# Kernel tuning notes

Measured on AMD Instinct MI355X. Metric: run time of the kernel, lower is better.

## Reference

```python
import jax, jax.numpy as jnp
import numpy as np

VAR_NUM = 96
EMBED_TIME = 128
INPUT_DIM = VAR_NUM * 2 + EMBED_TIME  # 320
ATTN_DIM = 64
N_HEADS = 8
ALL_DIM = ATTN_DIM * N_HEADS  # 512
B, N = 8, 2048
NEG_INF = -1e9  # finite stand-in for masked_fill(-inf); safe under softmax


def setup_inputs() -> dict:
    key = jax.random.key(0)
    ks = jax.random.split(key, 16)
    s = lambda d: 1.0 / np.sqrt(d)
    return {
        "times_in": jax.random.uniform(ks[0], (B, N), jnp.float32),
        "data_in": jax.random.normal(ks[1], (B, N, VAR_NUM), jnp.float32),
        "mask_in": jnp.ones((B, N, VAR_NUM), jnp.float32),
        "exist_times": jax.random.randint(ks[2], (B, N), 0, 2, jnp.int32),
        # TimeEmbedding params
        "w_per": jax.random.normal(ks[3], (1, EMBED_TIME - 1), jnp.float32),
        "b_per": jnp.zeros((EMBED_TIME - 1,), jnp.float32),
        "w_lin": jax.random.normal(ks[4], (1, 1), jnp.float32),
        "b_lin": jnp.zeros((1,), jnp.float32),
        # Attention params
        "Wq": jax.random.normal(ks[5], (INPUT_DIM, ALL_DIM), jnp.float32) * s(INPUT_DIM),
        "bq": jnp.zeros((ALL_DIM,), jnp.float32),
        "Wk": jax.random.normal(ks[6], (INPUT_DIM, ALL_DIM), jnp.float32) * s(INPUT_DIM),
        "bk": jnp.zeros((ALL_DIM,), jnp.float32),
        "Wv": jax.random.normal(ks[7], (INPUT_DIM, ALL_DIM), jnp.float32) * s(INPUT_DIM),
        "bv": jnp.zeros((ALL_DIM,), jnp.float32),
        "Wfc": jax.random.normal(ks[8], (ALL_DIM, ATTN_DIM), jnp.float32) * s(ALL_DIM),
        "bfc": jnp.zeros((ATTN_DIM,), jnp.float32),
    }


def reference(times_in, data_in, mask_in, exist_times,
              w_per, b_per, w_lin, b_lin,
              Wq, bq, Wk, bk, Wv, bv, Wfc, bfc):
    b, n = times_in.shape
    tt = times_in[..., None]  # [b, n, 1]
    # TimeEmbedding: [linear(tt), sin(periodic(tt))]
    te = jnp.concatenate([tt @ w_lin + b_lin, jnp.sin(tt @ w_per + b_per)], axis=-1)
    x = jnp.concatenate([data_in, mask_in, te], axis=-1)  # [b, n, INPUT_DIM]

    def heads(w, bias):
        return (x @ w + bias).reshape(b, n, N_HEADS, ATTN_DIM).transpose(0, 2, 1, 3)

    q, k, v = heads(Wq, bq), heads(Wk, bk), heads(Wv, bv)  # [b, h, n, d]
    # NOTE: custom scale uses sqrt(input_dim), not sqrt(head_dim)
    scores = jnp.einsum("bhqd,bhkd->bhqk", q, k) / jnp.sqrt(jnp.float32(INPUT_DIM))
    m = (exist_times != 0)
    scores = jnp.where(m[:, None, None, :], scores, NEG_INF)  # mask keys
    attn = jax.nn.softmax(scores, axis=-1)  # dropout p=0 in eval reference
    out = jnp.einsum("bhqk,bhkd->bhqd", attn, v)
    out = jnp.where(m[:, None, :, None], out, 0.0)  # zero masked query rows
    out = out.transpose(0, 2, 1, 3).reshape(b, n, ALL_DIM)
    return out @ Wfc + bfc  # [b, n, ATTN_DIM]
```

## Files before the change

### kernel.cpp

```cpp
#include <hip/hip_runtime.h>

#define N_ 2048
#define BN 16384
#define IN_DIM 320
#define QKV_N 1536
#define ALPHA 0.08064911f

typedef float f32x4 __attribute__((ext_vector_type(4)));
typedef short v8s __attribute__((ext_vector_type(8)));
typedef unsigned int u32x2 __attribute__((ext_vector_type(2)));

__device__ __forceinline__ short f2b(float f) {
  unsigned u = __builtin_bit_cast(unsigned, f);
  u = u + 0x7fff + ((u >> 16) & 1);
  return (short)(u >> 16);
}

__device__ __forceinline__ int piperm(int t) {
  return ((t >> 5) & 1) * 32 + ((t >> 2) & 3) * 8 + ((t >> 4) & 1) * 4 + (t & 3);
}

__device__ __forceinline__ size_t fragaddr(int ti, int r, int k) {
  return (size_t)ti * 512 + ((k >> 3) & 3) * 128 + r * 8 + (k & 7);
}

__global__ void build_x(const float* __restrict__ times, const float* __restrict__ data,
                        const float* __restrict__ maskv, const float* __restrict__ w_per,
                        const float* __restrict__ b_per, const float* __restrict__ w_lin,
                        const float* __restrict__ b_lin, short* __restrict__ xF) {
  int row = blockIdx.x;
  int t = threadIdx.x;
  float tt = times[row];
  int rt = row >> 4, l16r = row & 15;
  const float* dr = data + (size_t)row * 96;
  const float* mr = maskv + (size_t)row * 96;
  if (t < 96) {
    xF[fragaddr(rt * 10 + (t >> 5), l16r, t & 31)] = f2b(dr[t]);
    int k2 = 96 + t;
    xF[fragaddr(rt * 10 + (k2 >> 5), l16r, k2 & 31)] = f2b(mr[t]);
  }
  float val;
  if (t == 0) val = tt * w_lin[0] + b_lin[0];
  else        val = __sinf(tt * w_per[t - 1] + b_per[t - 1]);
  int k3 = 192 + t;
  xF[fragaddr(rt * 10 + (k3 >> 5), l16r, k3 & 31)] = f2b(val);
}

__global__ void scan_mask(const int* __restrict__ exist, int* __restrict__ prefix,
                          int* __restrict__ ntg, int* __restrict__ totals,
                          short* __restrict__ flagsc) {
  __shared__ int sums[256];
  int b = blockIdx.x;
  int t = threadIdx.x;
  const int* e = exist + b * 2048;
  int loc[8];
  int s = 0;
#pragma unroll
  for (int j = 0; j < 8; ++j) { loc[j] = s; s += (e[t * 8 + j] != 0) ? 1 : 0; }
  sums[t] = s;
  __syncthreads();
  for (int d = 1; d < 256; d <<= 1) {
    int v = (t >= d) ? sums[t - d] : 0;
    __syncthreads();
    sums[t] += v;
    __syncthreads();
  }
  int total = sums[255];
  int base = (t == 0) ? 0 : sums[t - 1];
#pragma unroll
  for (int j = 0; j < 8; ++j) prefix[b * 2048 + t * 8 + j] = base + loc[j];
  if (t == 0) { ntg[b] = (total + 63) >> 6; totals[b] = total; }
#pragma unroll
  for (int j = 0; j < 8; ++j) {
    int slot = t * 8 + j;
    flagsc[b * 2048 + (slot & ~63) + piperm(slot & 63)] =
        (slot < total) ? (short)0x3F80 : (short)0;
  }
}

__global__ void transpose_w(const float* __restrict__ Wq, const float* __restrict__ Wk,
                            const float* __restrict__ Wv, const float* __restrict__ Wfc,
                            short* __restrict__ WtF, short* __restrict__ WfcT) {
  int idx = blockIdx.x * 256 + threadIdx.x;
  if (idx < QKV_N * IN_DIM) {
    int n = idx / IN_DIM, kk = idx - n * IN_DIM;
    const float* W = (n < 512) ? Wq : (n < 1024 ? Wk : Wv);
    WtF[fragaddr((n >> 4) * 10 + (kk >> 5), n & 15, kk & 31)] =
        f2b(W[(size_t)kk * 512 + (n & 511)]);
  } else {
    int j = idx - QKV_N * IN_DIM;
    int d = j >> 9, kk = j & 511;
    WfcT[j] = f2b(Wfc[kk * 64 + d]);
  }
}

__launch_bounds__(256)
__global__ void qkv_gemm(const short* __restrict__ xF, const short* __restrict__ WtF,
                         const float* __restrict__ bq, const float* __restrict__ bk,
                         const float* __restrict__ bv, const int* __restrict__ exist,
                         const int* __restrict__ prefix,
                         short* __restrict__ q, short* __restrict__ kc, short* __restrict__ vc) {
  int bm = blockIdx.x;
  int bn = blockIdx.y;
  int tid = threadIdx.x, wave = tid >> 6, lane = tid & 63;
  int wm = wave >> 1, wn = wave & 1;
  int l16 = lane & 15, lh = lane >> 4;
  int voff = lane * 8;
  const short* ap = xF + (size_t)(bm * 8 + wm * 4) * 10 * 512;
  const short* bp = WtF + (size_t)(bn * 8 + wn * 4) * 10 * 512;
  f32x4 acc[4][4] = {};
  v8s af[4], bfr[4];
#pragma unroll
  for (int m = 0; m < 4; ++m) af[m] = *(const v8s*)&ap[(size_t)(m * 10) * 512 + voff];
#pragma unroll
  for (int n = 0; n < 4; ++n) bfr[n] = *(const v8s*)&bp[(size_t)(n * 10) * 512 + voff];
#pragma unroll 1
  for (int kt = 0; kt < 10; ++kt) {
#pragma unroll
    for (int m = 0; m < 4; ++m)
#pragma unroll
      for (int n = 0; n < 4; ++n)
        acc[m][n] = __builtin_amdgcn_mfma_f32_16x16x32_bf16(af[m], bfr[n], acc[m][n], 0, 0, 0);
    if (kt < 9) {
#pragma unroll
      for (int m = 0; m < 4; ++m) af[m] = *(const v8s*)&ap[(size_t)(m * 10 + kt + 1) * 512 + voff];
#pragma unroll
      for (int n = 0; n < 4; ++n) bfr[n] = *(const v8s*)&bp[(size_t)(n * 10 + kt + 1) * 512 + voff];
    }
  }
  int w = bn >> 2;
  if (w == 0) {
#pragma unroll
    for (int m = 0; m < 4; ++m) {
      int row0 = bm * 128 + wm * 64 + m * 16 + lh * 4;
#pragma unroll
      for (int n = 0; n < 4; ++n) {
        int c = (bn * 128 + wn * 64 + n * 16 + l16) & 511;
        float bb = bq[c];
        int h = c >> 6, d = c & 63;
#pragma unroll
        for (int r = 0; r < 4; ++r) {
          int rr = row0 + r;
          int b = rr >> 11, ntok = rr & 2047;
          q[(((size_t)(b * 8 + h) * N_ + ntok) << 6) + d] = f2b((acc[m][n][r] + bb) * ALPHA);
        }
      }
    }
  } else {
    short* dbuf = (w == 1) ? kc : vc;
    const float* bias = (w == 1) ? bk : bv;
#pragma unroll
    for (int m = 0; m < 4; ++m) {
      int row0 = bm * 128 + wm * 64 + m * 16 + lh * 4;
      int exr[4], dstr[4];
#pragma unroll
      for (int r = 0; r < 4; ++r) { exr[r] = exist[row0 + r]; dstr[r] = prefix[row0 + r]; }
      int b = row0 >> 11;
#pragma unroll
      for (int n = 0; n < 4; ++n) {
        int c = (bn * 128 + wn * 64 + n * 16 + l16) & 511;
        float bb = bias[c];
        int h = c >> 6, d = c & 63;
#pragma unroll
        for (int r = 0; r < 4; ++r)
          if (exr[r])
            dbuf[(((size_t)(b * 8 + h) * N_ + dstr[r]) << 6) + d] = f2b(acc[m][n][r] + bb);
      }
    }
  }
}

__launch_bounds__(256)
__global__ void fragmentize(short* __restrict__ kc, short* __restrict__ vc,
                            const int* __restrict__ ntg, const int* __restrict__ totals) {
  __shared__ short Ks[64][66];
  __shared__ short Vs[64][66];
  int bh = blockIdx.x;
  int b = bh >> 3;
  int nt = ntg[b], total = totals[b];
  int tid = threadIdx.x;
  size_t hb = (size_t)bh * N_ * 64;
  for (int tile = blockIdx.y; tile < nt; tile += 8) {
    int base = tile * 64;
#pragma unroll
    for (int s = 0; s < 2; ++s) {
      int c = tid + s * 256, r = c >> 3, c8 = c & 7;
      v8s kv = {0, 0, 0, 0, 0, 0, 0, 0};
      v8s vv = {0, 0, 0, 0, 0, 0, 0, 0};
      if (base + r < total) {
        kv = *(const v8s*)&kc[hb + (size_t)(base + r) * 64 + c8 * 8];
        vv = *(const v8s*)&vc[hb + (size_t)(base + r) * 64 + c8 * 8];
      }
      *(v8s*)&Ks[r][c8 * 8] = kv;
      *(v8s*)&Vs[r][c8 * 8] = vv;
    }
    __syncthreads();
#pragma unroll
    for (int s = 0; s < 2; ++s) {
      int c = tid + s * 256;
      int i = c >> 6, lh2 = (c >> 4) & 3, r16 = c & 15;
      *(v8s*)&kc[hb + (size_t)tile * 4096 + c * 8] =
          *(const v8s*)&Ks[(i >> 1) * 16 + r16][(i & 1) * 32 + lh2 * 8];
      int l16 = c & 15, lh = (c >> 4) & 3, kc2 = (c >> 6) & 1, n2 = c >> 7;
      int d = n2 * 16 + l16;
      v8s o;
#pragma unroll
      for (int jj = 0; jj < 8; ++jj) {
        int t2 = kc2 * 32 + (jj >> 2) * 16 + lh * 4 + (jj & 3);
        o[jj] = Vs[t2][d];
      }
      *(v8s*)&vc[hb + (size_t)tile * 4096 + c * 8] = o;
    }
    __syncthreads();
  }
}

__launch_bounds__(256, 2)
__global__ void attn_kernel(const short* __restrict__ q, const short* __restrict__ kT,
                            const short* __restrict__ vT, const short* __restrict__ flagsc,
                            const int* __restrict__ ntg, const int* __restrict__ exist,
                            short* __restrict__ att) {
  int bx = blockIdx.x;
  int bh = ((bx >> 6) << 3) | (bx & 7);
  int qblk = (bx >> 3) & 7;
  int b = bh >> 3, h = bh & 7;
  int tid = threadIdx.x, wave = tid >> 6, lane = tid & 63;
  int l16 = lane & 15, lh = lane >> 4;
  int q0 = qblk * 256 + wave * 64;
  int nt = ntg[b];
  const short* qp = q + (size_t)bh * N_ * 64;
  const short* kpt = kT + (size_t)bh * 131072;
  const short* vpt = vT + (size_t)bh * 131072;
  const short* fpt = flagsc + b * N_;
  const int* ex = exist + b * N_;
  v8s qf[4][2];
#pragma unroll
  for (int m = 0; m < 4; ++m)
#pragma unroll
    for (int kcx = 0; kcx < 2; ++kcx)
      qf[m][kcx] = *(const v8s*)&qp[(size_t)(q0 + m * 16 + l16) * 64 + kcx * 32 + lh * 8];
  f32x4 oacc[4][4] = {};
  f32x4 lacc[4] = {};
  const f32x4 zf = {0.f, 0.f, 0.f, 0.f};
  int voff = lane * 8;
  v8s kf[8], vf[8], ff[2];
#pragma unroll
  for (int i = 0; i < 8; ++i) {
    kf[i] = *(const v8s*)&kpt[i * 512 + voff];
    vf[i] = *(const v8s*)&vpt[i * 512 + voff];
  }
  ff[0] = *(const v8s*)&fpt[lh * 8];
  ff[1] = *(const v8s*)&fpt[32 + lh * 8];
#pragma unroll 1
  for (int kt = 0; kt < nt; ++kt) {
    const short* kn = kpt + (size_t)(kt + 1) * 4096;
    const short* vn = vpt + (size_t)(kt + 1) * 4096;
    const short* fn = fpt + (kt + 1) * 64;
    bool pre = (kt + 1 < nt);
#pragma unroll
    for (int mh = 0; mh < 2; ++mh) {
      f32x4 sacc[2][4];
#pragma unroll
      for (int n = 0; n < 4; ++n)
#pragma unroll
        for (int mm = 0; mm < 2; ++mm) {
          sacc[mm][n] = __builtin_amdgcn_mfma_f32_16x16x32_bf16(kf[n * 2], qf[mh * 2 + mm][0], zf, 0, 0, 0);
          sacc[mm][n] = __builtin_amdgcn_mfma_f32_16x16x32_bf16(kf[n * 2 + 1], qf[mh * 2 + mm][1], sacc[mm][n], 0, 0, 0);
        }
      if (mh == 1 && pre)
#pragma unroll
        for (int i = 0; i < 8; ++i) kf[i] = *(const v8s*)&kn[i * 512 + voff];
      v8s pf[2][2];
#pragma unroll
      for (int mm = 0; mm < 2; ++mm)
#pragma unroll
        for (int kcx = 0; kcx < 2; ++kcx)
#pragma unroll
          for (int half = 0; half < 2; ++half) {
            int n = kcx * 2 + half;
            float p0 = __builtin_amdgcn_exp2f(sacc[mm][n][0]);
            float p1 = __builtin_amdgcn_exp2f(sacc[mm][n][1]);
            float p2 = __builtin_amdgcn_exp2f(sacc[mm][n][2]);
            float p3 = __builtin_amdgcn_exp2f(sacc[mm][n][3]);
            uint w0, w1;
            asm("v_cvt_pk_bf16_f32 %0, %1, %2" : "=v"(w0) : "v"(p0), "v"(p1));
            asm("v_cvt_pk_bf16_f32 %0, %1, %2" : "=v"(w1) : "v"(p2), "v"(p3));
            ((uint*)&pf[mm][kcx])[half * 2]     = w0;
            ((uint*)&pf[mm][kcx])[half * 2 + 1] = w1;
          }
#pragma unroll
      for (int kcx = 0; kcx < 2; ++kcx) {
#pragma unroll
        for (int mm = 0; mm < 2; ++mm)
          lacc[mh * 2 + mm] = __builtin_amdgcn_mfma_f32_16x16x32_bf16(pf[mm][kcx], ff[kcx], lacc[mh * 2 + mm], 0, 0, 0);
#pragma unroll
        for (int n = 0; n < 4; ++n)
#pragma unroll
          for (int mm = 0; mm < 2; ++mm)
            oacc[mh * 2 + mm][n] = __builtin_amdgcn_mfma_f32_16x16x32_bf16(pf[mm][kcx], vf[n * 2 + kcx], oacc[mh * 2 + mm][n], 0, 0, 0);
      }
    }
    if (pre) {
#pragma unroll
      for (int i = 0; i < 8; ++i) vf[i] = *(const v8s*)&vn[i * 512 + voff];
      ff[0] = *(const v8s*)&fn[lh * 8];
      ff[1] = *(const v8s*)&fn[32 + lh * 8];
    }
  }
#pragma unroll
  for (int m = 0; m < 4; ++m)
#pragma unroll
    for (int r = 0; r < 4; ++r) {
      int row = q0 + m * 16 + lh * 4 + r;
      float qm = (ex[row] != 0) ? 1.f : 0.f;
      float inv = qm / fmaxf(lacc[m][r], 1e-20f);
#pragma unroll
      for (int n = 0; n < 4; ++n)
        att[((size_t)(b * N_ + row)) * 512 + h * 64 + n * 16 + l16] = f2b(oacc[m][n][r] * inv);
    }
}

__launch_bounds__(256)
__global__ void out_gemm(const short* __restrict__ att, const short* __restrict__ WfcT,
                         const float* __restrict__ bfc, float* __restrict__ out) {
  __shared__ short As[128][40];
  __shared__ short Bs[64][40];
  int bm = blockIdx.x;
  int tid = threadIdx.x, wave = tid >> 6, lane = tid & 63;
  int l16 = lane & 15, lh = lane >> 4;
  f32x4 acc[2][4] = {};
  for (int kt = 0; kt < 16; ++kt) {
    int k0 = kt * 32;
#pragma unroll
    for (int s = 0; s < 2; ++s) {
      int c = tid + s * 256;
      int r = c >> 2, c8 = c & 3;
      *(v8s*)&As[r][c8 * 8] = *(const v8s*)&att[(size_t)(bm * 128 + r) * 512 + k0 + c8 * 8];
    }
    { int r = tid >> 2, c8 = tid & 3;
      if (r < 64) *(v8s*)&Bs[r][c8 * 8] = *(const v8s*)&WfcT[(size_t)r * 512 + k0 + c8 * 8]; }
    __syncthreads();
    v8s bfr[4];
#pragma unroll
    for (int n = 0; n < 4; ++n) bfr[n] = *(const v8s*)&Bs[n * 16 + l16][lh * 8];
#pragma unroll
    for (int m = 0; m < 2; ++m) {
      v8s af = *(const v8s*)&As[wave * 32 + m * 16 + l16][lh * 8];
#pragma unroll
      for (int n = 0; n < 4; ++n)
        acc[m][n] = __builtin_amdgcn_mfma_f32_16x16x32_bf16(af, bfr[n], acc[m][n], 0, 0, 0);
    }
    __syncthreads();
  }
#pragma unroll
  for (int m = 0; m < 2; ++m)
#pragma unroll
    for (int n = 0; n < 4; ++n) {
      float bb = bfc[n * 16 + l16];
#pragma unroll
      for (int r = 0; r < 4; ++r) {
        int row = bm * 128 + wave * 32 + m * 16 + lh * 4 + r;
        out[(size_t)row * 64 + n * 16 + l16] = acc[m][n][r] + bb;
      }
    }
}

extern "C" void kernel_launch(void* const* d_in, const int* in_sizes, int n_in,
                              void* d_out, int out_size, void* d_ws, size_t ws_size,
                              hipStream_t stream) {
  const float* times = (const float*)d_in[0];
  const float* data  = (const float*)d_in[1];
  const float* maskv = (const float*)d_in[2];
  const int*   exist = (const int*)d_in[3];
  const float* w_per = (const float*)d_in[4];
  const float* b_per = (const float*)d_in[5];
  const float* w_lin = (const float*)d_in[6];
  const float* b_lin = (const float*)d_in[7];
  const float* Wq  = (const float*)d_in[8];
  const float* bq  = (const float*)d_in[9];
  const float* Wk  = (const float*)d_in[10];
  const float* bk  = (const float*)d_in[11];
  const float* Wv  = (const float*)d_in[12];
  const float* bv  = (const float*)d_in[13];
  const float* Wfc = (const float*)d_in[14];
  const float* bfc = (const float*)d_in[15];
  float* out = (float*)d_out;

  char* ws = (char*)d_ws;
  short* xF    = (short*)(ws);
  short* WtF   = (short*)(ws + 10485760);
  short* WfcT  = (short*)(ws + 11468800);
  short* qb    = (short*)(ws + 11534336);
  short* kcb   = (short*)(ws + 28311552);
  short* vcb   = (short*)(ws + 45088768);
  short* att   = (short*)(ws + 61865984);
  short* flagsc= (short*)(ws + 78643200);
  int*   prefix= (int*)(ws + 78675968);
  int*   ntg   = (int*)(ws + 78741504);
  int*   totals= (int*)(ws + 78741536);

  build_x<<<BN, 128, 0, stream>>>(times, data, maskv, w_per, b_per, w_lin, b_lin, xF);
  scan_mask<<<8, 256, 0, stream>>>(exist, prefix, ntg, totals, flagsc);
  transpose_w<<<2048, 256, 0, stream>>>(Wq, Wk, Wv, Wfc, WtF, WfcT);
  qkv_gemm<<<dim3(128, 12), 256, 0, stream>>>(xF, WtF, bq, bk, bv, exist, prefix, qb, kcb, vcb);
  fragmentize<<<dim3(64, 8), 256, 0, stream>>>(kcb, vcb, ntg, totals);
  attn_kernel<<<512, 256, 0, stream>>>(qb, kcb, vcb, flagsc, ntg, exist, att);
  out_gemm<<<128, 256, 0, stream>>>(att, WfcT, bfc, out);
}
```

Baseline: 109.6 us.

## Compact existing rows before K/V GEMM and drop key-flag vectors in attention

build_x now also writes a compacted copy of the input rows, placed using the prefix scan, so the K/V projection GEMM runs only over existing tokens. Row blocks past each batch's valid count exit early, which removes roughly the masked fraction of K/V projection work and the scattered prefix/exist lookups in its epilogue. The attention kernel no longer loads per-tile flag vectors: it computes the row sum with a constant ones vector and subtracts the padding count from the denominator. This relies on padded K/V slots being zeroed later, so each pad contributes exactly exp2(0)=1 to the sum. The compacted buffer reuses the att workspace region, and scan_mask must now run before build_x.

```diff
diff --git a/kernel.cpp b/kernel.cpp
--- a/kernel.cpp
+++ b/kernel.cpp
@@ -24,31 +24,8 @@
   return (size_t)ti * 512 + ((k >> 3) & 3) * 128 + r * 8 + (k & 7);
 }
 
-__global__ void build_x(const float* __restrict__ times, const float* __restrict__ data,
-                        const float* __restrict__ maskv, const float* __restrict__ w_per,
-                        const float* __restrict__ b_per, const float* __restrict__ w_lin,
-                        const float* __restrict__ b_lin, short* __restrict__ xF) {
-  int row = blockIdx.x;
-  int t = threadIdx.x;
-  float tt = times[row];
-  int rt = row >> 4, l16r = row & 15;
-  const float* dr = data + (size_t)row * 96;
-  const float* mr = maskv + (size_t)row * 96;
-  if (t < 96) {
-    xF[fragaddr(rt * 10 + (t >> 5), l16r, t & 31)] = f2b(dr[t]);
-    int k2 = 96 + t;
-    xF[fragaddr(rt * 10 + (k2 >> 5), l16r, k2 & 31)] = f2b(mr[t]);
-  }
-  float val;
-  if (t == 0) val = tt * w_lin[0] + b_lin[0];
-  else        val = __sinf(tt * w_per[t - 1] + b_per[t - 1]);
-  int k3 = 192 + t;
-  xF[fragaddr(rt * 10 + (k3 >> 5), l16r, k3 & 31)] = f2b(val);
-}
-
 __global__ void scan_mask(const int* __restrict__ exist, int* __restrict__ prefix,
-                          int* __restrict__ ntg, int* __restrict__ totals,
-                          short* __restrict__ flagsc) {
+                          int* __restrict__ ntg, int* __restrict__ totals) {
   __shared__ int sums[256];
   int b = blockIdx.x;
   int t = threadIdx.x;
@@ -70,12 +47,42 @@
 #pragma unroll
   for (int j = 0; j < 8; ++j) prefix[b * 2048 + t * 8 + j] = base + loc[j];
   if (t == 0) { ntg[b] = (total + 63) >> 6; totals[b] = total; }
-#pragma unroll
-  for (int j = 0; j < 8; ++j) {
-    int slot = t * 8 + j;
-    flagsc[b * 2048 + (slot & ~63) + piperm(slot & 63)] =
-        (slot < total) ? (short)0x3F80 : (short)0;
-  }
+}
+
+__global__ void build_x(const float* __restrict__ times, const float* __restrict__ data,
+                        const float* __restrict__ maskv, const float* __restrict__ w_per,
+                        const float* __restrict__ b_per, const float* __restrict__ w_lin,
+                        const float* __restrict__ b_lin, const int* __restrict__ exist,
+                        const int* __restrict__ prefix,
+                        short* __restrict__ xF, short* __restrict__ xFc) {
+  int row = blockIdx.x;
+  int t = threadIdx.x;
+  float tt = times[row];
+  int rt = row >> 4, l16r = row & 15;
+  int b = row >> 11;
+  int dst = prefix[row];
+  bool ex = exist[row] != 0;
+  int tcb = (b * 128 + (dst >> 4)) * 10;
+  int l16c = dst & 15;
+  const float* dr = data + (size_t)row * 96;
+  const float* mr = maskv + (size_t)row * 96;
+  if (t < 96) {
+    short v1 = f2b(dr[t]), v2 = f2b(mr[t]);
+    int k2 = 96 + t;
+    xF[fragaddr(rt * 10 + (t >> 5), l16r, t & 31)] = v1;
+    xF[fragaddr(rt * 10 + (k2 >> 5), l16r, k2 & 31)] = v2;
+    if (ex) {
+      xFc[fragaddr(tcb + (t >> 5), l16c, t & 31)] = v1;
+      xFc[fragaddr(tcb + (k2 >> 5), l16c, k2 & 31)] = v2;
+    }
+  }
+  float val;
+  if (t == 0) val = tt * w_lin[0] + b_lin[0];
+  else        val = __sinf(tt * w_per[t - 1] + b_per[t - 1]);
+  int k3 = 192 + t;
+  short v3 = f2b(val);
+  xF[fragaddr(rt * 10 + (k3 >> 5), l16r, k3 & 31)] = v3;
+  if (ex) xFc[fragaddr(tcb + (k3 >> 5), l16c, k3 & 31)] = v3;
 }
 
 __global__ void transpose_w(const float* __restrict__ Wq, const float* __restrict__ Wk,
@@ -95,18 +102,22 @@
 }
 
 __launch_bounds__(256)
-__global__ void qkv_gemm(const short* __restrict__ xF, const short* __restrict__ WtF,
+__global__ void qkv_gemm(const short* __restrict__ xF, const short* __restrict__ xFc,
+                         const short* __restrict__ WtF,
                          const float* __restrict__ bq, const float* __restrict__ bk,
-                         const float* __restrict__ bv, const int* __restrict__ exist,
-                         const int* __restrict__ prefix,
+                         const float* __restrict__ bv, const int* __restrict__ totals,
                          short* __restrict__ q, short* __restrict__ kc, short* __restrict__ vc) {
   int bm = blockIdx.x;
   int bn = blockIdx.y;
+  int w = bn >> 2;
+  int bb = bm >> 4, bq16 = bm & 15;
+  if (w != 0 && bq16 * 128 >= totals[bb]) return;
   int tid = threadIdx.x, wave = tid >> 6, lane = tid & 63;
   int wm = wave >> 1, wn = wave & 1;
   int l16 = lane & 15, lh = lane >> 4;
   int voff = lane * 8;
-  const short* ap = xF + (size_t)(bm * 8 + wm * 4) * 10 * 512;
+  const short* ap = (w == 0) ? xF + (size_t)(bm * 8 + wm * 4) * 10 * 512
+                             : xFc + (size_t)(bb * 128 + bq16 * 8 + wm * 4) * 10 * 512;
   const short* bp = WtF + (size_t)(bn * 8 + wn * 4) * 10 * 512;
   f32x4 acc[4][4] = {};
   v8s af[4], bfr[4];
@@ -128,7 +139,6 @@
       for (int n = 0; n < 4; ++n) bfr[n] = *(const v8s*)&bp[(size_t)(n * 10 + kt + 1) * 512 + voff];
     }
   }
-  int w = bn >> 2;
   if (w == 0) {
 #pragma unroll
     for (int m = 0; m < 4; ++m) {
@@ -136,13 +146,13 @@
 #pragma unroll
       for (int n = 0; n < 4; ++n) {
         int c = (bn * 128 + wn * 64 + n * 16 + l16) & 511;
-        float bb = bq[c];
+        float bb2 = bq[c];
         int h = c >> 6, d = c & 63;
 #pragma unroll
         for (int r = 0; r < 4; ++r) {
           int rr = row0 + r;
           int b = rr >> 11, ntok = rr & 2047;
-          q[(((size_t)(b * 8 + h) * N_ + ntok) << 6) + d] = f2b((acc[m][n][r] + bb) * ALPHA);
+          q[(((size_t)(b * 8 + h) * N_ + ntok) << 6) + d] = f2b((acc[m][n][r] + bb2) * ALPHA);
         }
       }
     }
@@ -151,20 +161,15 @@
     const float* bias = (w == 1) ? bk : bv;
 #pragma unroll
     for (int m = 0; m < 4; ++m) {
-      int row0 = bm * 128 + wm * 64 + m * 16 + lh * 4;
-      int exr[4], dstr[4];
-#pragma unroll
-      for (int r = 0; r < 4; ++r) { exr[r] = exist[row0 + r]; dstr[r] = prefix[row0 + r]; }
-      int b = row0 >> 11;
+      int crow0 = bq16 * 128 + wm * 64 + m * 16 + lh * 4;
 #pragma unroll
       for (int n = 0; n < 4; ++n) {
-        int c = (bn * 128 + wn * 64 + n * 16 + l16) & 511;
-        float bb = bias[c];
+        int c = ((bn & 3) * 128 + wn * 64 + n * 16 + l16);
+        float bb2 = bias[c];
         int h = c >> 6, d = c & 63;
 #pragma unroll
         for (int r = 0; r < 4; ++r)
-          if (exr[r])
-            dbuf[(((size_t)(b * 8 + h) * N_ + dstr[r]) << 6) + d] = f2b(acc[m][n][r] + bb);
+          dbuf[(((size_t)(bb * 8 + h) * N_ + crow0 + r) << 6) + d] = f2b(acc[m][n][r] + bb2);
       }
     }
   }
@@ -217,8 +222,8 @@
 
 __launch_bounds__(256, 2)
 __global__ void attn_kernel(const short* __restrict__ q, const short* __restrict__ kT,
-                            const short* __restrict__ vT, const short* __restrict__ flagsc,
-                            const int* __restrict__ ntg, const int* __restrict__ exist,
+                            const short* __restrict__ vT, const int* __restrict__ ntg,
+                            const int* __restrict__ totals, const int* __restrict__ exist,
                             short* __restrict__ att) {
   int bx = blockIdx.x;
   int bh = ((bx >> 6) << 3) | (bx & 7);
@@ -228,10 +233,10 @@
   int l16 = lane & 15, lh = lane >> 4;
   int q0 = qblk * 256 + wave * 64;
   int nt = ntg[b];
+  float padf = (float)(nt * 64 - totals[b]);
   const short* qp = q + (size_t)bh * N_ * 64;
   const short* kpt = kT + (size_t)bh * 131072;
   const short* vpt = vT + (size_t)bh * 131072;
-  const short* fpt = flagsc + b * N_;
   const int* ex = exist + b * N_;
   v8s qf[4][2];
 #pragma unroll
@@ -242,20 +247,20 @@
   f32x4 oacc[4][4] = {};
   f32x4 lacc[4] = {};
   const f32x4 zf = {0.f, 0.f, 0.f, 0.f};
+  v8s ones;
+#pragma unroll
+  for (int j = 0; j < 8; ++j) ones[j] = (short)0x3F80;
   int voff = lane * 8;
-  v8s kf[8], vf[8], ff[2];
+  v8s kf[8], vf[8];
 #pragma unroll
   for (int i = 0; i < 8; ++i) {
     kf[i] = *(const v8s*)&kpt[i * 512 + voff];
     vf[i] = *(const v8s*)&vpt[i * 512 + voff];
   }
-  ff[0] = *(const v8s*)&fpt[lh * 8];
-  ff[1] = *(const v8s*)&fpt[32 + lh * 8];
 #pragma unroll 1
   for (int kt = 0; kt < nt; ++kt) {
     const short* kn = kpt + (size_t)(kt + 1) * 4096;
     const short* vn = vpt + (size_t)(kt + 1) * 4096;
-    const short* fn = fpt + (kt + 1) * 64;
     bool pre = (kt + 1 < nt);
 #pragma unroll
     for (int mh = 0; mh < 2; ++mh) {
@@ -292,7 +297,7 @@
       for (int kcx = 0; kcx < 2; ++kcx) {
 #pragma unroll
         for (int mm = 0; mm < 2; ++mm)
-          lacc[mh * 2 + mm] = __builtin_amdgcn_mfma_f32_16x16x32_bf16(pf[mm][kcx], ff[kcx], lacc[mh * 2 + mm], 0, 0, 0);
+          lacc[mh * 2 + mm] = __builtin_amdgcn_mfma_f32_16x16x32_bf16(pf[mm][kcx], ones, lacc[mh * 2 + mm], 0, 0, 0);
 #pragma unroll
         for (int n = 0; n < 4; ++n)
 #pragma unroll
@@ -303,8 +308,6 @@
     if (pre) {
 #pragma unroll
       for (int i = 0; i < 8; ++i) vf[i] = *(const v8s*)&vn[i * 512 + voff];
-      ff[0] = *(const v8s*)&fn[lh * 8];
-      ff[1] = *(const v8s*)&fn[32 + lh * 8];
     }
   }
 #pragma unroll
@@ -313,7 +316,7 @@
     for (int r = 0; r < 4; ++r) {
       int row = q0 + m * 16 + lh * 4 + r;
       float qm = (ex[row] != 0) ? 1.f : 0.f;
-      float inv = qm / fmaxf(lacc[m][r], 1e-20f);
+      float inv = qm / fmaxf(lacc[m][r] - padf, 1e-20f);
 #pragma unroll
       for (int n = 0; n < 4; ++n)
         att[((size_t)(b * N_ + row)) * 512 + h * 64 + n * 16 + l16] = f2b(oacc[m][n][r] * inv);
@@ -394,16 +397,17 @@
   short* kcb   = (short*)(ws + 28311552);
   short* vcb   = (short*)(ws + 45088768);
   short* att   = (short*)(ws + 61865984);
-  short* flagsc= (short*)(ws + 78643200);
+  short* xFc   = (short*)(ws + 61865984);
   int*   prefix= (int*)(ws + 78675968);
   int*   ntg   = (int*)(ws + 78741504);
   int*   totals= (int*)(ws + 78741536);
 
-  build_x<<<BN, 128, 0, stream>>>(times, data, maskv, w_per, b_per, w_lin, b_lin, xF);
-  scan_mask<<<8, 256, 0, stream>>>(exist, prefix, ntg, totals, flagsc);
+  scan_mask<<<8, 256, 0, stream>>>(exist, prefix, ntg, totals);
+  build_x<<<BN, 128, 0, stream>>>(times, data, maskv, w_per, b_per, w_lin, b_lin,
+                                  exist, prefix, xF, xFc);
   transpose_w<<<2048, 256, 0, stream>>>(Wq, Wk, Wv, Wfc, WtF, WfcT);
-  qkv_gemm<<<dim3(128, 12), 256, 0, stream>>>(xF, WtF, bq, bk, bv, exist, prefix, qb, kcb, vcb);
+  qkv_gemm<<<dim3(128, 12), 256, 0, stream>>>(xF, xFc, WtF, bq, bk, bv, totals, qb, kcb, vcb);
   fragmentize<<<dim3(64, 8), 256, 0, stream>>>(kcb, vcb, ntg, totals);
-  attn_kernel<<<512, 256, 0, stream>>>(qb, kcb, vcb, flagsc, ntg, exist, att);
+  attn_kernel<<<512, 256, 0, stream>>>(qb, kcb, vcb, ntg, totals, exist, att);
   out_gemm<<<128, 256, 0, stream>>>(att, WfcT, bfc, out);
 }
```

Result: no change. 109.6 us (-0.0%).
